# Kernel tuning notes

Measured on AMD Instinct MI355X. Metric: run time of the kernel, lower is better.

The kernel has to match this reference:

```python
import jax, jax.numpy as jnp
import numpy as np

L, B, S, D, H, V = 6, 4, 1024, 1024, 16, 32000
HD = D // H          # head_size = 64
F = 4 * D            # ffn hidden
EPS = 1e-5           # nn.LayerNorm default


def setup_inputs() -> dict:
    key = jax.random.key(0)
    ks = jax.random.split(key, 12)
    s = 0.02
    p = {
        "tokens": jax.random.randint(ks[0], (B, S), 0, V, dtype=jnp.int32),
        "tok_emb": s * jax.random.normal(ks[1], (V, D), jnp.float32),
        "pos_emb": s * jax.random.normal(ks[2], (S, D), jnp.float32),
        # stacked per-layer params (leading dim L)
        "Wq": s * jax.random.normal(ks[3], (L, D, D), jnp.float32),
        "Wk": s * jax.random.normal(ks[4], (L, D, D), jnp.float32),
        "Wv": s * jax.random.normal(ks[5], (L, D, D), jnp.float32),
        "Wp": s * jax.random.normal(ks[6], (L, D, D), jnp.float32),
        "ln1_s": jnp.ones((L, D), jnp.float32),
        "ln1_b": jnp.zeros((L, D), jnp.float32),
        "W1": s * jax.random.normal(ks[7], (L, D, F), jnp.float32),
        "b1": jnp.zeros((L, F), jnp.float32),
        "W2": s * jax.random.normal(ks[8], (L, F, D), jnp.float32),
        "b2": jnp.zeros((L, D), jnp.float32),
        "ln2_s": jnp.ones((L, D), jnp.float32),
        "ln2_b": jnp.zeros((L, D), jnp.float32),
        "lnf_s": jnp.ones((D,), jnp.float32),
        "lnf_b": jnp.zeros((D,), jnp.float32),
        "Wh": s * jax.random.normal(ks[9], (D, V), jnp.float32),
        "bh": jnp.zeros((V,), jnp.float32),
    }
    return p


def _ln(x, scale, bias):
    m = x.mean(-1, keepdims=True)
    v = ((x - m) ** 2).mean(-1, keepdims=True)
    return (x - m) * jax.lax.rsqrt(v + EPS) * scale + bias


def reference(tokens, tok_emb, pos_emb, Wq, Wk, Wv, Wp, ln1_s, ln1_b,
              W1, b1, W2, b2, ln2_s, ln2_b, lnf_s, lnf_b, Wh, bh):
    x = tok_emb[tokens] + pos_emb[None, :, :]            # [B,S,D]
    mask = jnp.tril(jnp.ones((S, S), dtype=bool))
    inv_sqrt_hd = HD ** -0.5

    def layer(x, p):
        wq, wk, wv, wp, l1s, l1b, w1, b1_, w2, b2_, l2s, l2b = p
        q = jnp.einsum('bsd,dhk->bhsk', x, wq.reshape(D, H, HD))
        k = jnp.einsum('bsd,dhk->bhsk', x, wk.reshape(D, H, HD))
        v = jnp.einsum('bsd,dhk->bhsk', x, wv.reshape(D, H, HD))
        scores = jnp.einsum('bhsk,bhtk->bhst', q, k)     # [B,H,S,S]
        # original: masked_fill(-inf) THEN * head_size**-0.5 (same math: -inf stays -inf)
        scores = jnp.where(mask, scores * inv_sqrt_hd, -jnp.inf)
        attn = jax.nn.softmax(scores, axis=-1)
        o = jnp.einsum('bhst,bhtk->bhsk', attn, v)
        o = o.transpose(0, 2, 1, 3).reshape(B, S, D) @ wp
        a = x + _ln(o, l1s, l1b)                          # residual + ln1 (as in source)
        f = jax.nn.relu(a @ w1 + b1_) @ w2 + b2_
        return x + _ln(f, l2s, l2b), None                 # residual from block INPUT (as in source)

    x, _ = jax.lax.scan(layer, x,
                        (Wq, Wk, Wv, Wp, ln1_s, ln1_b, W1, b1, W2, b2, ln2_s, ln2_b))
    return _ln(x, lnf_s, lnf_b) @ Wh + bh                 # [B,S,V]
```

## Files before the change

### kernel.cpp

```cpp
#include <hip/hip_runtime.h>

#define DEV __device__ __forceinline__

typedef __attribute__((ext_vector_type(4))) float f32x4;
typedef __attribute__((ext_vector_type(8))) short short8_t;

constexpr int LNUM = 6;
constexpr int BB = 4;
constexpr int SS = 1024;
constexpr int DD = 1024;
constexpr int HH = 16;
constexpr int HDD = 64;
constexpr int FF = 4096;
constexpr int VV = 32000;
constexpr int MROWS = BB * SS;

DEV short f2bf(float f) {
  union { float f; unsigned u; } x; x.f = f;
  unsigned r = x.u + 0x7fffu + ((x.u >> 16) & 1u);
  return (short)(r >> 16);
}

#define BAR() do { __builtin_amdgcn_sched_barrier(0); \
  __builtin_amdgcn_s_barrier(); \
  __builtin_amdgcn_sched_barrier(0); } while (0)

__global__ __launch_bounds__(256) void k_embed(
    const int* __restrict__ tok, const float* __restrict__ te,
    const float* __restrict__ pe, float* __restrict__ xf,
    short* __restrict__ xb) {
  int i = blockIdx.x * 256 + threadIdx.x;
  int bs = i >> 8, d4 = i & 255;
  int t = tok[bs];
  float4 a = ((const float4*)(te + (size_t)t * DD))[d4];
  float4 b = ((const float4*)(pe + (size_t)(bs & (SS - 1)) * DD))[d4];
  float4 r; r.x = a.x + b.x; r.y = a.y + b.y; r.z = a.z + b.z; r.w = a.w + b.w;
  ((float4*)xf)[i] = r;
  short4 o; o.x = f2bf(r.x); o.y = f2bf(r.y); o.z = f2bf(r.z); o.w = f2bf(r.w);
  ((short4*)xb)[i] = o;
}

__global__ __launch_bounds__(256) void k_tcvt(
    const float* __restrict__ in, short* __restrict__ out, int K, int N,
    long long ostride) {
  __shared__ float tile[32][33];
  const float* ip = in + (size_t)blockIdx.z * K * N;
  short* op = out + (size_t)blockIdx.z * ostride;
  int bn = blockIdx.x * 32, bk = blockIdx.y * 32;
  int tx = threadIdx.x, ty = threadIdx.y;
  #pragma unroll
  for (int r = 0; r < 32; r += 8)
    tile[ty + r][tx] = ip[(size_t)(bk + ty + r) * N + bn + tx];
  __syncthreads();
  #pragma unroll
  for (int r = 0; r < 32; r += 8)
    op[(size_t)(bn + ty + r) * K + bk + tx] = f2bf(tile[tx][ty + r]);
}

DEV void gload16(const short* g, short* l) {
  __builtin_amdgcn_global_load_lds(
      (const __attribute__((address_space(1))) void*)g,
      (__attribute__((address_space(3))) void*)l, 16, 0, 0);
}

template<int MODE>
__global__ __launch_bounds__(512, 2) void k_gemm256(
    const short* __restrict__ A, const short* __restrict__ Bt,
    const float* __restrict__ bias, void* __restrict__ Cp,
    int M, int N, int K, int lda, int ldb) {
  extern __shared__ short lds[];
  const int tid = threadIdx.x;
  const int nbx = gridDim.x;
  const int nwg = nbx << 4;
  const int hid = blockIdx.y * nbx + blockIdx.x;
  const int cpx = nwg >> 3;
  const int lid = (hid & 7) * cpx + (hid >> 3);
  const int bx = lid >> 4, by = lid & 15;
  const int n0 = bx * 256, m0 = by * 256;

  const int lane = tid & 63;
  const int wid = tid >> 6;
  const int wm = wid >> 2, wn = wid & 3;
  const int l16 = lane & 15, kg = lane >> 4;
  const int xorv = (l16 & 7) << 4;
  const int cs[2] = { ((kg << 4) ^ xorv) >> 1,
                      ((64 | (kg << 4)) ^ xorv) >> 1 };
  const int rr = tid >> 3;
  const int sce = ((((tid & 7) << 4) ^ ((rr & 7) << 4)) >> 1);
  const int ldst = (tid & ~63) * 8;

  const int NT = K >> 6;

  auto stageA = [&](int t2, int c2) {
    const int k0 = t2 << 6;
    const int base = c2 * 32768;
    #pragma unroll
    for (int h = 0; h < 2; h++)
      #pragma unroll
      for (int li = 0; li < 2; li++)
        gload16(A + (size_t)(m0 + h * 128 + li * 64 + rr) * lda + k0 + sce,
                &lds[base + h * 8192 + li * 4096 + ldst]);
  };
  auto stageB = [&](int t2, int c2) {
    const int k0 = t2 << 6;
    const int base = c2 * 32768 + 16384;
    #pragma unroll
    for (int h = 0; h < 2; h++)
      #pragma unroll
      for (int li = 0; li < 2; li++)
        gload16(Bt + (size_t)(n0 + h * 128 + li * 64 + rr) * ldb + k0 + sce,
                &lds[base + h * 8192 + li * 4096 + ldst]);
  };

  f32x4 acc[8][4];
  #pragma unroll
  for (int mi = 0; mi < 8; mi++)
    #pragma unroll
    for (int ni = 0; ni < 4; ni++)
      #pragma unroll
      for (int j = 0; j < 4; j++) acc[mi][ni][j] = 0.f;

  auto storeQ = [&](int mlo, int nlo) {
    #pragma unroll
    for (int mi = 0; mi < 4; mi++)
      #pragma unroll
      for (int ni = 0; ni < 2; ni++)
        #pragma unroll
        for (int j = 0; j < 4; j++) {
          const int r = m0 + wm * 128 + (mlo + mi) * 16 + kg * 4 + j;
          const int c = n0 + wn * 64 + (nlo + ni) * 16 + l16;
          ((float*)Cp)[(size_t)r * N + c] = acc[mlo + mi][nlo + ni][j] + bias[c];
        }
  };

  stageA(0, 0); stageB(0, 0);
  stageA(1, 1); stageB(1, 1);
  asm volatile("s_waitcnt vmcnt(8)" ::: "memory");
  BAR();

  for (int t = 0; t < NT; t++) {
    const int c = t & 1;
    const int ao = c * 32768 + wm * 8192;
    const int bo = c * 32768 + 16384 + (wn >> 1) * 8192 + (wn & 1) * 4096;
    short8_t a[4][2], b0[2][2], b1[2][2];

    #pragma unroll
    for (int mi = 0; mi < 4; mi++)
      #pragma unroll
      for (int kk = 0; kk < 2; kk++)
        a[mi][kk] = *(const short8_t*)&lds[ao + (mi * 16 + l16) * 64 + cs[kk]];
    #pragma unroll
    for (int ni = 0; ni < 2; ni++)
      #pragma unroll
      for (int kk = 0; kk < 2; kk++)
        b0[ni][kk] = *(const short8_t*)&lds[bo + (ni * 16 + l16) * 64 + cs[kk]];
    BAR();
    __builtin_amdgcn_s_setprio(1);
    #pragma unroll
    for (int mi = 0; mi < 4; mi++)
      #pragma unroll
      for (int ni = 0; ni < 2; ni++)
        #pragma unroll
        for (int kk = 0; kk < 2; kk++)
          acc[mi][ni] = __builtin_amdgcn_mfma_f32_16x16x32_bf16(
              a[mi][kk], b0[ni][kk], acc[mi][ni], 0, 0, 0);
    __builtin_amdgcn_s_setprio(0);
    if (MODE == 9 && t == NT - 1) storeQ(0, 0);
    BAR();

    #pragma unroll
    for (int ni = 0; ni < 2; ni++)
      #pragma unroll
      for (int kk = 0; kk < 2; kk++)
        b1[ni][kk] = *(const short8_t*)&lds[bo + ((ni + 2) * 16 + l16) * 64 + cs[kk]];
    BAR();
    __builtin_amdgcn_s_setprio(1);
    #pragma unroll
    for (int mi = 0; mi < 4; mi++)
      #pragma unroll
      for (int ni = 0; ni < 2; ni++)
        #pragma unroll
        for (int kk = 0; kk < 2; kk++)
          acc[mi][ni + 2] = __builtin_amdgcn_mfma_f32_16x16x32_bf16(
              a[mi][kk], b1[ni][kk], acc[mi][ni + 2], 0, 0, 0);
    __builtin_amdgcn_s_setprio(0);
    if (MODE == 9 && t == NT - 1) storeQ(0, 2);
    BAR();

    #pragma unroll
    for (int mi = 0; mi < 4; mi++)
      #pragma unroll
      for (int kk = 0; kk < 2; kk++)
        a[mi][kk] = *(const short8_t*)&lds[ao + ((mi + 4) * 16 + l16) * 64 + cs[kk]];
    if (t + 2 < NT) stageB(t + 2, c);
    BAR();
    __builtin_amdgcn_s_setprio(1);
    #pragma unroll
    for (int mi = 0; mi < 4; mi++)
      #pragma unroll
      for (int ni = 0; ni < 2; ni++)
        #pragma unroll
        for (int kk = 0; kk < 2; kk++)
          acc[mi + 4][ni + 2] = __builtin_amdgcn_mfma_f32_16x16x32_bf16(
              a[mi][kk], b1[ni][kk], acc[mi + 4][ni + 2], 0, 0, 0);
    __builtin_amdgcn_s_setprio(0);
    if (MODE == 9 && t == NT - 1) storeQ(4, 2);
    BAR();

    if (t + 2 < NT) stageA(t + 2, c);
    BAR();
    __builtin_amdgcn_s_setprio(1);
    #pragma unroll
    for (int mi = 0; mi < 4; mi++)
      #pragma unroll
      for (int ni = 0; ni < 2; ni++)
        #pragma unroll
        for (int kk = 0; kk < 2; kk++)
          acc[mi + 4][ni] = __builtin_amdgcn_mfma_f32_16x16x32_bf16(
              a[mi][kk], b0[ni][kk], acc[mi + 4][ni], 0, 0, 0);
    __builtin_amdgcn_s_setprio(0);
    if (t + 2 < NT) asm volatile("s_waitcnt vmcnt(8)" ::: "memory");
    else            asm volatile("s_waitcnt vmcnt(0)" ::: "memory");
    BAR();
  }

  if (MODE == 9) {
    storeQ(4, 0);
    return;
  }
  #pragma unroll
  for (int mi = 0; mi < 8; mi++) {
    #pragma unroll
    for (int ni = 0; ni < 4; ni++) {
      #pragma unroll
      for (int j = 0; j < 4; j++) {
        const int r = m0 + wm * 128 + mi * 16 + kg * 4 + j;
        const int c = n0 + wn * 64 + ni * 16 + l16;
        const float v = acc[mi][ni][j];
        if (MODE == 6) {
          ((short*)Cp)[(size_t)r * N + c] = f2bf(fmaxf(v + bias[c], 0.f));
        } else if (MODE == 8) {
          int kind = c >> 10, cc = c & 1023;
          int b = r >> 10, s = r & 1023, h = cc >> 6, hd = cc & 63;
          size_t off;
          if (kind < 2)
            off = (size_t)kind * MROWS * DD +
                  (((size_t)(b * HH + h) << 10) + s) * HDD + hd;
          else
            off = (size_t)2 * MROWS * DD +
                  (((size_t)(b * HH + h) * HDD + hd) << 10) + s;
          ((short*)Cp)[off] = f2bf(v);
        }
      }
    }
  }
}

template<int MODE>
__global__ __launch_bounds__(256) void k_gemm(
    const short* __restrict__ A, const short* __restrict__ Bt,
    const float* __restrict__ bias, void* __restrict__ Cp,
    int M, int N, int K, int lda, int ldb) {
  __shared__ short lA[4096];
  __shared__ short lB[4096];
  const int tid = threadIdx.x;
  const int n0 = blockIdx.x * 128, m0 = blockIdx.y * 128;

  const int lane = tid & 63;
  const int wm = (tid >> 6) >> 1, wn = (tid >> 6) & 1;
  const int l16 = lane & 15, kg = lane >> 4;
  const int srow = tid >> 2, scol = (tid & 3) * 8;
  const int lbase = (tid & ~63) * 8;

  f32x4 acc[4][4];
  #pragma unroll
  for (int a = 0; a < 4; a++)
    #pragma unroll
    for (int b = 0; b < 4; b++)
      #pragma unroll
      for (int j = 0; j < 4; j++) acc[a][b][j] = 0.f;

  for (int k0 = 0; k0 < K; k0 += 32) {
    #pragma unroll
    for (int i = 0; i < 2; i++)
      gload16(A + (size_t)(m0 + i * 64 + srow) * lda + (k0 + scol),
              &lA[i * 2048 + lbase]);
    #pragma unroll
    for (int i = 0; i < 2; i++)
      gload16(Bt + (size_t)(n0 + i * 64 + srow) * ldb + (k0 + scol),
              &lB[i * 2048 + lbase]);
    __syncthreads();
    short8_t af[4], bf[4];
    #pragma unroll
    for (int mi = 0; mi < 4; mi++)
      af[mi] = *(const short8_t*)&lA[(wm * 64 + mi * 16 + l16) * 32 + kg * 8];
    #pragma unroll
    for (int ni = 0; ni < 4; ni++)
      bf[ni] = *(const short8_t*)&lB[(wn * 64 + ni * 16 + l16) * 32 + kg * 8];
    #pragma unroll
    for (int mi = 0; mi < 4; mi++)
      #pragma unroll
      for (int ni = 0; ni < 4; ni++)
        acc[mi][ni] = __builtin_amdgcn_mfma_f32_16x16x32_bf16(
            af[mi], bf[ni], acc[mi][ni], 0, 0, 0);
    __syncthreads();
  }

  #pragma unroll
  for (int mi = 0; mi < 4; mi++) {
    #pragma unroll
    for (int ni = 0; ni < 4; ni++) {
      #pragma unroll
      for (int j = 0; j < 4; j++) {
        const int r = m0 + wm * 64 + mi * 16 + kg * 4 + j;
        const int c = n0 + wn * 64 + ni * 16 + l16;
        const float v = acc[mi][ni][j];
        if (MODE == 5) {
          ((float*)Cp)[(size_t)r * N + c] = v;
        } else if (MODE == 7) {
          ((float*)Cp)[(size_t)r * N + c] = v + bias[c];
        }
      }
    }
  }
}

#define RDSWZ(arr, r, cb) \
  (*(const short8_t*)&arr[((r) << 6) + ((((cb) ^ (((r) & 7) << 4))) >> 1)])
#define RDSWZ7(arr, r, cb) \
  (*(const short8_t*)&arr[((r) << 7) + ((((cb) ^ (((r) & 7) << 4))) >> 1)])

__global__ __launch_bounds__(512, 2) void k_attn(
    const short* __restrict__ Qg, const short* __restrict__ Kgl,
    const short* __restrict__ Vt, short* __restrict__ Og) {
  extern __shared__ short sm[];
  short* lP = sm + 32768;
  const int tid = threadIdx.x;
  const int z = blockIdx.y;
  const int qb = (z < 32) ? blockIdx.x : 7 - blockIdx.x;
  const int q0 = qb << 7;
  const short* Qp = Qg + ((size_t)z << 16);
  const short* Kp = Kgl + ((size_t)z << 16);
  const short* Vp = Vt + ((size_t)z << 16);
  const int bidx = z >> 4, h = z & 15;
  const int lane = tid & 63, w = tid >> 6;
  const int l16 = lane & 15, kg = lane >> 4;
  const int sr = tid >> 3;
  const int scb = ((((tid & 7) << 4) ^ ((sr & 7) << 4)) >> 1);
  const int vr = tid >> 4;
  const int vcb = ((((tid & 15) << 4) ^ ((vr & 7) << 4)) >> 1);
  const int ldst = (tid & ~63) << 3;

  auto stageK = [&](int kt, int c) {
    const int k0 = kt << 7;
    short* dst = sm + c * 16384;
    #pragma unroll
    for (int i = 0; i < 2; i++)
      gload16(Kp + ((size_t)(k0 + i * 64 + sr) << 6) + scb,
              dst + i * 4096 + ldst);
  };
  auto stageV = [&](int kt, int c) {
    const int k0 = kt << 7;
    short* dst = sm + c * 16384 + 8192;
    #pragma unroll
    for (int i = 0; i < 2; i++)
      gload16(Vp + ((size_t)(i * 32 + vr) << 10) + k0 + vcb,
              dst + i * 4096 + ldst);
  };

  #pragma unroll
  for (int i = 0; i < 2; i++)
    gload16(Qp + ((size_t)(q0 + i * 64 + sr) << 6) + scb,
            sm + 16384 + i * 4096 + ldst);
  __syncthreads();
  short8_t aq[2];
  #pragma unroll
  for (int kk = 0; kk < 2; kk++)
    aq[kk] = RDSWZ((sm + 16384), w * 16 + l16, kk * 64 + kg * 16);
  __syncthreads();

  f32x4 acc_o[4];
  float m_r[4], l_r[4];
  #pragma unroll
  for (int j = 0; j < 4; j++) {
    m_r[j] = -3e38f; l_r[j] = 0.f;
    #pragma unroll
    for (int n2 = 0; n2 < 4; n2++) acc_o[n2][j] = 0.f;
  }

  const float C = 0.125f * 1.44269504f;
  const int nkt = qb + 1;
  stageK(0, 0); stageV(0, 0);

  for (int kt = 0; kt < nkt; kt++) {
    const int cur = kt & 1;
    if (kt + 1 < nkt) {
      stageK(kt + 1, cur ^ 1); stageV(kt + 1, cur ^ 1);
      asm volatile("s_waitcnt vmcnt(4)" ::: "memory");
    } else {
      asm volatile("s_waitcnt vmcnt(0)" ::: "memory");
    }
    BAR();

    const short* lK = sm + cur * 16384;
    const short* lV = sm + cur * 16384 + 8192;
    const int k0 = kt << 7;

    f32x4 s[8];
    #pragma unroll
    for (int nf = 0; nf < 8; nf++)
      #pragma unroll
      for (int j = 0; j < 4; j++) s[nf][j] = 0.f;
    #pragma unroll
    for (int kk = 0; kk < 2; kk++)
      #pragma unroll
      for (int nf = 0; nf < 8; nf++) {
        short8_t bk = RDSWZ(lK, nf * 16 + l16, kk * 64 + kg * 16);
        s[nf] = __builtin_amdgcn_mfma_f32_16x16x32_bf16(aq[kk], bk, s[nf], 0, 0, 0);
      }

    const bool diag = (kt == qb);
    #pragma unroll
    for (int j = 0; j < 4; j++) {
      const int ql = w * 16 + kg * 4 + j;
      const int q = q0 + ql;
      float sv[8]; float tm = -3e38f;
      #pragma unroll
      for (int nf = 0; nf < 8; nf++) {
        const int kv = k0 + nf * 16 + l16;
        const float x = s[nf][j] * C;
        sv[nf] = (!diag || kv <= q) ? x : -3e38f;
        tm = fmaxf(tm, sv[nf]);
      }
      #pragma unroll
      for (int o = 1; o < 16; o <<= 1) tm = fmaxf(tm, __shfl_xor(tm, o));
      const float mn = fmaxf(m_r[j], tm);
      const float scale = exp2f(m_r[j] - mn);
      float ts = 0.f;
      #pragma unroll
      for (int nf = 0; nf < 8; nf++) {
        const float e = exp2f(sv[nf] - mn);
        ts += e;
        lP[(ql << 7) + ((nf * 16 + l16) ^ ((ql & 7) << 3))] = f2bf(e);
      }
      #pragma unroll
      for (int o = 1; o < 16; o <<= 1) ts += __shfl_xor(ts, o);
      l_r[j] = l_r[j] * scale + ts;
      m_r[j] = mn;
      #pragma unroll
      for (int n2 = 0; n2 < 4; n2++) acc_o[n2][j] *= scale;
    }

    #pragma unroll
    for (int kc = 0; kc < 4; kc++) {
      const int pr = w * 16 + l16;
      short8_t pa = *(const short8_t*)
          &lP[(pr << 7) + ((kc * 32 + kg * 8) ^ ((pr & 7) << 3))];
      #pragma unroll
      for (int n2 = 0; n2 < 4; n2++) {
        short8_t vb = RDSWZ7(lV, n2 * 16 + l16, kc * 64 + kg * 16);
        acc_o[n2] = __builtin_amdgcn_mfma_f32_16x16x32_bf16(pa, vb, acc_o[n2], 0, 0, 0);
      }
    }
    BAR();
  }

  #pragma unroll
  for (int j = 0; j < 4; j++) {
    const int q = q0 + w * 16 + kg * 4 + j;
    const float inv = 1.f / l_r[j];
    #pragma unroll
    for (int n2 = 0; n2 < 4; n2++) {
      const int col = h * HDD + n2 * 16 + l16;
      Og[(((size_t)bidx << 10) + q) * DD + col] = f2bf(acc_o[n2][j] * inv);
    }
  }
}

template<int ADD_RES, int WRITE_F32>
__global__ __launch_bounds__(256) void k_ln(
    const float* __restrict__ src, const float* __restrict__ res,
    const float* __restrict__ g, const float* __restrict__ b,
    float* __restrict__ of, short* __restrict__ ob) {
  const int row = blockIdx.x;
  const int tid = threadIdx.x;
  float4 v = ((const float4*)(src + ((size_t)row << 10)))[tid];
  float s1 = v.x + v.y + v.z + v.w;
  float s2 = v.x * v.x + v.y * v.y + v.z * v.z + v.w * v.w;
  #pragma unroll
  for (int o = 32; o; o >>= 1) { s1 += __shfl_xor(s1, o); s2 += __shfl_xor(s2, o); }
  __shared__ float sh1[4], sh2[4];
  if ((tid & 63) == 0) { sh1[tid >> 6] = s1; sh2[tid >> 6] = s2; }
  __syncthreads();
  s1 = sh1[0] + sh1[1] + sh1[2] + sh1[3];
  s2 = sh2[0] + sh2[1] + sh2[2] + sh2[3];
  const float mean = s1 * (1.f / 1024.f);
  const float var  = s2 * (1.f / 1024.f) - mean * mean;
  const float rs = rsqrtf(var + 1e-5f);
  float4 gg = ((const float4*)g)[tid];
  float4 bb = ((const float4*)b)[tid];
  float4 o4;
  o4.x = (v.x - mean) * rs * gg.x + bb.x;
  o4.y = (v.y - mean) * rs * gg.y + bb.y;
  o4.z = (v.z - mean) * rs * gg.z + bb.z;
  o4.w = (v.w - mean) * rs * gg.w + bb.w;
  if (ADD_RES) {
    float4 rr = ((const float4*)(res + ((size_t)row << 10)))[tid];
    o4.x += rr.x; o4.y += rr.y; o4.z += rr.z; o4.w += rr.w;
  }
  if (WRITE_F32) ((float4*)(of + ((size_t)row << 10)))[tid] = o4;
  short4 s4; s4.x = f2bf(o4.x); s4.y = f2bf(o4.y);
  s4.z = f2bf(o4.z); s4.w = f2bf(o4.w);
  ((short4*)ob)[((size_t)row << 8) + tid] = s4;
}

extern "C" void kernel_launch(void* const* d_in, const int* in_sizes, int n_in,
                              void* d_out, int out_size, void* d_ws, size_t ws_size,
                              hipStream_t stream) {
  (void)in_sizes; (void)n_in; (void)out_size; (void)ws_size;
  const int*   tokens  = (const int*)d_in[0];
  const float* tok_emb = (const float*)d_in[1];
  const float* pos_emb = (const float*)d_in[2];
  const float* Wq = (const float*)d_in[3];
  const float* Wk = (const float*)d_in[4];
  const float* Wv = (const float*)d_in[5];
  const float* Wp = (const float*)d_in[6];
  const float* ln1s = (const float*)d_in[7];
  const float* ln1b = (const float*)d_in[8];
  const float* W1 = (const float*)d_in[9];
  const float* b1 = (const float*)d_in[10];
  const float* W2 = (const float*)d_in[11];
  const float* b2 = (const float*)d_in[12];
  const float* ln2s = (const float*)d_in[13];
  const float* ln2b = (const float*)d_in[14];
  const float* lnfs = (const float*)d_in[15];
  const float* lnfb = (const float*)d_in[16];
  const float* Wh = (const float*)d_in[17];
  const float* bh = (const float*)d_in[18];
  float* out = (float*)d_out;

  hipFuncSetAttribute((const void*)k_gemm256<6>,
      hipFuncAttributeMaxDynamicSharedMemorySize, 131072);
  hipFuncSetAttribute((const void*)k_gemm256<8>,
      hipFuncAttributeMaxDynamicSharedMemorySize, 131072);
  hipFuncSetAttribute((const void*)k_gemm256<9>,
      hipFuncAttributeMaxDynamicSharedMemorySize, 131072);
  hipFuncSetAttribute((const void*)k_attn,
      hipFuncAttributeMaxDynamicSharedMemorySize, 98304);

  char* p = (char*)d_ws;
  auto alloc = [&](size_t elems, size_t esz) -> char* {
    char* r = p; p += (elems * esz + 255) & ~(size_t)255; return r;
  };
  short* WqkvT = (short*)alloc((size_t)LNUM * 3 * DD * DD, 2);
  short* WpT = (short*)alloc((size_t)LNUM * DD * DD, 2);
  short* W1T = (short*)alloc((size_t)LNUM * DD * FF, 2);
  short* W2T = (short*)alloc((size_t)LNUM * DD * FF, 2);
  short* WhT = (short*)alloc((size_t)DD * VV, 2);
  float* xf   = (float*)alloc((size_t)MROWS * DD, 4);
  float* ff   = (float*)alloc((size_t)MROWS * DD, 4);
  short* xb   = (short*)alloc((size_t)MROWS * DD, 2);
  short* ab   = (short*)alloc((size_t)MROWS * DD, 2);
  short* qkvb = (short*)alloc((size_t)3 * MROWS * DD, 2);
  short* obuf = (short*)alloc((size_t)MROWS * DD, 2);
  short* hb   = (short*)alloc((size_t)MROWS * FF, 2);
  short* xfb  = (short*)alloc((size_t)MROWS * DD, 2);
  short* qb   = qkvb;
  short* kb   = qkvb + (size_t)MROWS * DD;
  short* vtb  = qkvb + (size_t)2 * MROWS * DD;

  dim3 blk(256);
  dim3 t8(32, 8);
  const long long DD2 = (long long)DD * DD;
  k_tcvt<<<dim3(DD / 32, DD / 32, LNUM), t8, 0, stream>>>(Wq, WqkvT,          DD, DD, 3 * DD2);
  k_tcvt<<<dim3(DD / 32, DD / 32, LNUM), t8, 0, stream>>>(Wk, WqkvT + DD2,    DD, DD, 3 * DD2);
  k_tcvt<<<dim3(DD / 32, DD / 32, LNUM), t8, 0, stream>>>(Wv, WqkvT + 2*DD2,  DD, DD, 3 * DD2);
  k_tcvt<<<dim3(DD / 32, DD / 32, LNUM), t8, 0, stream>>>(Wp, WpT, DD, DD, DD2);
  k_tcvt<<<dim3(FF / 32, DD / 32, LNUM), t8, 0, stream>>>(W1, W1T, DD, FF, (long long)DD * FF);
  k_tcvt<<<dim3(DD / 32, FF / 32, LNUM), t8, 0, stream>>>(W2, W2T, FF, DD, (long long)DD * FF);
  k_tcvt<<<dim3(VV / 32, DD / 32, 1),   t8, 0, stream>>>(Wh, WhT, DD, VV, 0);

  k_embed<<<(MROWS * DD / 4) / 256, blk, 0, stream>>>(tokens, tok_emb, pos_emb, xf, xb);

  for (int l = 0; l < LNUM; l++) {
    const short* wqkv = WqkvT + (size_t)l * 3 * DD * DD;
    const short* wp = WpT + (size_t)l * DD * DD;
    const short* w1 = W1T + (size_t)l * DD * FF;
    const short* w2 = W2T + (size_t)l * DD * FF;

    k_gemm256<8><<<dim3(12, 16), 512, 131072, stream>>>(xb, wqkv, nullptr, qkvb,
        MROWS, 3 * DD, DD, DD, DD);
    k_attn<<<dim3(8, BB * HH), 512, 98304, stream>>>(qb, kb, vtb, obuf);
    k_gemm<5><<<dim3(8, 32), blk, 0, stream>>>(obuf, wp, nullptr, ff,
        MROWS, DD, DD, DD, DD);
    k_ln<1, 0><<<MROWS, blk, 0, stream>>>(ff, xf, ln1s + (size_t)l * DD,
        ln1b + (size_t)l * DD, nullptr, ab);
    k_gemm256<6><<<dim3(16, 16), 512, 131072, stream>>>(ab, w1, b1 + (size_t)l * FF, hb,
        MROWS, FF, DD, DD, DD);
    k_gemm<7><<<dim3(8, 32), blk, 0, stream>>>(hb, w2, b2 + (size_t)l * DD, ff,
        MROWS, DD, FF, FF, FF);
    k_ln<1, 1><<<MROWS, blk, 0, stream>>>(ff, xf, ln2s + (size_t)l * DD,
        ln2b + (size_t)l * DD, xf, xb);
  }

  k_ln<0, 0><<<MROWS, blk, 0, stream>>>(xf, nullptr, lnfs, lnfb, nullptr, xfb);
  k_gemm256<9><<<dim3(VV / 256, 16), 512, 131072, stream>>>(xfb, WhT, bh, out,
      MROWS, VV, DD, DD, DD);
}
```

Before: 2.398 ms.

## Replace 256x256 GEMM with 256x128 tile, BK=32 kernel for more occupancy

Replaces the 256x256-tile, K=64, four-phase interleaved GEMM with a simpler 256x128 tile over 32-wide K steps. It uses one combined A/B stage per iteration and 48KB of LDS, so up to four blocks can fit per CU. The grids for the QKV, FFN1 and LM-head GEMMs double, which improves wave balance on the many CUs. The cost is lower arithmetic intensity per tile, more barriers per unit of K, and loss of the fine-grained load/MFMA interleaving. It also merges the three Q/K/V weight transpose launches into one kernel.

```diff
diff --git a/kernel.cpp b/kernel.cpp
--- a/kernel.cpp
+++ b/kernel.cpp
@@ -57,6 +57,25 @@
     op[(size_t)(bn + ty + r) * K + bk + tx] = f2bf(tile[tx][ty + r]);
 }
 
+__global__ __launch_bounds__(256) void k_tcvt3(
+    const float* __restrict__ Wq, const float* __restrict__ Wk,
+    const float* __restrict__ Wv, short* __restrict__ out) {
+  __shared__ float tile[32][33];
+  const int z = blockIdx.z, l = z / 3, which = z - l * 3;
+  const float* ip = (which == 0 ? Wq : which == 1 ? Wk : Wv)
+                    + (size_t)l * DD * DD;
+  short* op = out + ((size_t)l * 3 + which) * DD * DD;
+  int bn = blockIdx.x * 32, bk = blockIdx.y * 32;
+  int tx = threadIdx.x, ty = threadIdx.y;
+  #pragma unroll
+  for (int r = 0; r < 32; r += 8)
+    tile[ty + r][tx] = ip[(size_t)(bk + ty + r) * DD + bn + tx];
+  __syncthreads();
+  #pragma unroll
+  for (int r = 0; r < 32; r += 8)
+    op[(size_t)(bn + ty + r) * DD + bk + tx] = f2bf(tile[tx][ty + r]);
+}
+
 DEV void gload16(const short* g, short* l) {
   __builtin_amdgcn_global_load_lds(
       (const __attribute__((address_space(1))) void*)g,
@@ -64,7 +83,7 @@
 }
 
 template<int MODE>
-__global__ __launch_bounds__(512, 2) void k_gemm256(
+__global__ __launch_bounds__(512, 4) void k_g2(
     const short* __restrict__ A, const short* __restrict__ Bt,
     const float* __restrict__ bias, void* __restrict__ Cp,
     int M, int N, int K, int lda, int ldb) {
@@ -76,169 +95,81 @@
   const int cpx = nwg >> 3;
   const int lid = (hid & 7) * cpx + (hid >> 3);
   const int bx = lid >> 4, by = lid & 15;
-  const int n0 = bx * 256, m0 = by * 256;
+  const int n0 = bx * 128, m0 = by * 256;
 
   const int lane = tid & 63;
   const int wid = tid >> 6;
-  const int wm = wid >> 2, wn = wid & 3;
+  const int wm = wid >> 1, wn = wid & 1;
   const int l16 = lane & 15, kg = lane >> 4;
-  const int xorv = (l16 & 7) << 4;
-  const int cs[2] = { ((kg << 4) ^ xorv) >> 1,
-                      ((64 | (kg << 4)) ^ xorv) >> 1 };
-  const int rr = tid >> 3;
-  const int sce = ((((tid & 7) << 4) ^ ((rr & 7) << 4)) >> 1);
+  const int cso = ((kg << 4) ^ ((l16 & 3) << 4)) >> 1;
+  const int rr = tid >> 2;
+  const int sce = ((((tid & 3) << 4) ^ ((rr & 3) << 4)) >> 1);
   const int ldst = (tid & ~63) * 8;
 
-  const int NT = K >> 6;
-
-  auto stageA = [&](int t2, int c2) {
-    const int k0 = t2 << 6;
-    const int base = c2 * 32768;
+  const int NT = K >> 5;
+
+  auto stage = [&](int t2, int c) {
+    const int k0 = t2 << 5;
     #pragma unroll
     for (int h = 0; h < 2; h++)
-      #pragma unroll
-      for (int li = 0; li < 2; li++)
-        gload16(A + (size_t)(m0 + h * 128 + li * 64 + rr) * lda + k0 + sce,
-                &lds[base + h * 8192 + li * 4096 + ldst]);
+      gload16(A + (size_t)(m0 + h * 128 + rr) * lda + k0 + sce,
+              &lds[c * 12288 + h * 4096 + ldst]);
+    gload16(Bt + (size_t)(n0 + rr) * ldb + k0 + sce,
+            &lds[c * 12288 + 8192 + ldst]);
   };
-  auto stageB = [&](int t2, int c2) {
-    const int k0 = t2 << 6;
-    const int base = c2 * 32768 + 16384;
-    #pragma unroll
-    for (int h = 0; h < 2; h++)
-      #pragma unroll
-      for (int li = 0; li < 2; li++)
-        gload16(Bt + (size_t)(n0 + h * 128 + li * 64 + rr) * ldb + k0 + sce,
-                &lds[base + h * 8192 + li * 4096 + ldst]);
-  };
-
-  f32x4 acc[8][4];
-  #pragma unroll
-  for (int mi = 0; mi < 8; mi++)
+
+  f32x4 acc[4][4];
+  #pragma unroll
+  for (int mi = 0; mi < 4; mi++)
     #pragma unroll
     for (int ni = 0; ni < 4; ni++)
       #pragma unroll
       for (int j = 0; j < 4; j++) acc[mi][ni][j] = 0.f;
 
-  auto storeQ = [&](int mlo, int nlo) {
-    #pragma unroll
-    for (int mi = 0; mi < 4; mi++)
-      #pragma unroll
-      for (int ni = 0; ni < 2; ni++)
-        #pragma unroll
-        for (int j = 0; j < 4; j++) {
-          const int r = m0 + wm * 128 + (mlo + mi) * 16 + kg * 4 + j;
-          const int c = n0 + wn * 64 + (nlo + ni) * 16 + l16;
-          ((float*)Cp)[(size_t)r * N + c] = acc[mlo + mi][nlo + ni][j] + bias[c];
-        }
-  };
-
-  stageA(0, 0); stageB(0, 0);
-  stageA(1, 1); stageB(1, 1);
-  asm volatile("s_waitcnt vmcnt(8)" ::: "memory");
+  stage(0, 0); stage(1, 1);
+  asm volatile("s_waitcnt vmcnt(3)" ::: "memory");
   BAR();
 
   for (int t = 0; t < NT; t++) {
     const int c = t & 1;
-    const int ao = c * 32768 + wm * 8192;
-    const int bo = c * 32768 + 16384 + (wn >> 1) * 8192 + (wn & 1) * 4096;
-    short8_t a[4][2], b0[2][2], b1[2][2];
-
+    const int ab = c * 12288;
+    short8_t a[4], b[4];
     #pragma unroll
     for (int mi = 0; mi < 4; mi++)
-      #pragma unroll
-      for (int kk = 0; kk < 2; kk++)
-        a[mi][kk] = *(const short8_t*)&lds[ao + (mi * 16 + l16) * 64 + cs[kk]];
-    #pragma unroll
-    for (int ni = 0; ni < 2; ni++)
-      #pragma unroll
-      for (int kk = 0; kk < 2; kk++)
-        b0[ni][kk] = *(const short8_t*)&lds[bo + (ni * 16 + l16) * 64 + cs[kk]];
+      a[mi] = *(const short8_t*)&lds[ab + (wm * 64 + mi * 16 + l16) * 32 + cso];
+    #pragma unroll
+    for (int ni = 0; ni < 4; ni++)
+      b[ni] = *(const short8_t*)&lds[ab + 8192 + (wn * 64 + ni * 16 + l16) * 32 + cso];
+    asm volatile("s_waitcnt lgkmcnt(0)" ::: "memory");
+    __builtin_amdgcn_sched_barrier(0);
     BAR();
+    if (t + 2 < NT) stage(t + 2, c);
     __builtin_amdgcn_s_setprio(1);
     #pragma unroll
     for (int mi = 0; mi < 4; mi++)
       #pragma unroll
-      for (int ni = 0; ni < 2; ni++)
-        #pragma unroll
-        for (int kk = 0; kk < 2; kk++)
-          acc[mi][ni] = __builtin_amdgcn_mfma_f32_16x16x32_bf16(
-              a[mi][kk], b0[ni][kk], acc[mi][ni], 0, 0, 0);
+      for (int ni = 0; ni < 4; ni++)
+        acc[mi][ni] = __builtin_amdgcn_mfma_f32_16x16x32_bf16(
+            a[mi], b[ni], acc[mi][ni], 0, 0, 0);
     __builtin_amdgcn_s_setprio(0);
-    if (MODE == 9 && t == NT - 1) storeQ(0, 0);
+    if (t + 2 < NT)      asm volatile("s_waitcnt vmcnt(3)" ::: "memory");
+    else if (t + 1 < NT) asm volatile("s_waitcnt vmcnt(0)" ::: "memory");
     BAR();
-
-    #pragma unroll
-    for (int ni = 0; ni < 2; ni++)
-      #pragma unroll
-      for (int kk = 0; kk < 2; kk++)
-        b1[ni][kk] = *(const short8_t*)&lds[bo + ((ni + 2) * 16 + l16) * 64 + cs[kk]];
-    BAR();
-    __builtin_amdgcn_s_setprio(1);
-    #pragma unroll
-    for (int mi = 0; mi < 4; mi++)
-      #pragma unroll
-      for (int ni = 0; ni < 2; ni++)
-        #pragma unroll
-        for (int kk = 0; kk < 2; kk++)
-          acc[mi][ni + 2] = __builtin_amdgcn_mfma_f32_16x16x32_bf16(
-              a[mi][kk], b1[ni][kk], acc[mi][ni + 2], 0, 0, 0);
-    __builtin_amdgcn_s_setprio(0);
-    if (MODE == 9 && t == NT - 1) storeQ(0, 2);
-    BAR();
-
-    #pragma unroll
-    for (int mi = 0; mi < 4; mi++)
-      #pragma unroll
-      for (int kk = 0; kk < 2; kk++)
-        a[mi][kk] = *(const short8_t*)&lds[ao + ((mi + 4) * 16 + l16) * 64 + cs[kk]];
-    if (t + 2 < NT) stageB(t + 2, c);
-    BAR();
-    __builtin_amdgcn_s_setprio(1);
-    #pragma unroll
-    for (int mi = 0; mi < 4; mi++)
-      #pragma unroll
-      for (int ni = 0; ni < 2; ni++)
-        #pragma unroll
-        for (int kk = 0; kk < 2; kk++)
-          acc[mi + 4][ni + 2] = __builtin_amdgcn_mfma_f32_16x16x32_bf16(
-              a[mi][kk], b1[ni][kk], acc[mi + 4][ni + 2], 0, 0, 0);
-    __builtin_amdgcn_s_setprio(0);
-    if (MODE == 9 && t == NT - 1) storeQ(4, 2);
-    BAR();
-
-    if (t + 2 < NT) stageA(t + 2, c);
-    BAR();
-    __builtin_amdgcn_s_setprio(1);
-    #pragma unroll
-    for (int mi = 0; mi < 4; mi++)
-      #pragma unroll
-      for (int ni = 0; ni < 2; ni++)
-        #pragma unroll
-        for (int kk = 0; kk < 2; kk++)
-          acc[mi + 4][ni] = __builtin_amdgcn_mfma_f32_16x16x32_bf16(
-              a[mi][kk], b0[ni][kk], acc[mi + 4][ni], 0, 0, 0);
-    __builtin_amdgcn_s_setprio(0);
-    if (t + 2 < NT) asm volatile("s_waitcnt vmcnt(8)" ::: "memory");
-    else            asm volatile("s_waitcnt vmcnt(0)" ::: "memory");
-    BAR();
-  }
-
-  if (MODE == 9) {
-    storeQ(4, 0);
-    return;
-  }
-  #pragma unroll
-  for (int mi = 0; mi < 8; mi++) {
+  }
+
+  #pragma unroll
+  for (int mi = 0; mi < 4; mi++) {
     #pragma unroll
     for (int ni = 0; ni < 4; ni++) {
       #pragma unroll
       for (int j = 0; j < 4; j++) {
-        const int r = m0 + wm * 128 + mi * 16 + kg * 4 + j;
+        const int r = m0 + wm * 64 + mi * 16 + kg * 4 + j;
         const int c = n0 + wn * 64 + ni * 16 + l16;
         const float v = acc[mi][ni][j];
         if (MODE == 6) {
           ((short*)Cp)[(size_t)r * N + c] = f2bf(fmaxf(v + bias[c], 0.f));
+        } else if (MODE == 9) {
+          ((float*)Cp)[(size_t)r * N + c] = v + bias[c];
         } else if (MODE == 8) {
           int kind = c >> 10, cc = c & 1023;
           int b = r >> 10, s = r & 1023, h = cc >> 6, hd = cc & 63;
@@ -539,12 +470,12 @@
   const float* bh = (const float*)d_in[18];
   float* out = (float*)d_out;
 
-  hipFuncSetAttribute((const void*)k_gemm256<6>,
-      hipFuncAttributeMaxDynamicSharedMemorySize, 131072);
-  hipFuncSetAttribute((const void*)k_gemm256<8>,
-      hipFuncAttributeMaxDynamicSharedMemorySize, 131072);
-  hipFuncSetAttribute((const void*)k_gemm256<9>,
-      hipFuncAttributeMaxDynamicSharedMemorySize, 131072);
+  hipFuncSetAttribute((const void*)k_g2<6>,
+      hipFuncAttributeMaxDynamicSharedMemorySize, 49152);
+  hipFuncSetAttribute((const void*)k_g2<8>,
+      hipFuncAttributeMaxDynamicSharedMemorySize, 49152);
+  hipFuncSetAttribute((const void*)k_g2<9>,
+      hipFuncAttributeMaxDynamicSharedMemorySize, 49152);
   hipFuncSetAttribute((const void*)k_attn,
       hipFuncAttributeMaxDynamicSharedMemorySize, 98304);
 
@@ -571,13 +502,13 @@
 
   dim3 blk(256);
   dim3 t8(32, 8);
-  const long long DD2 = (long long)DD * DD;
-  k_tcvt<<<dim3(DD / 32, DD / 32, LNUM), t8, 0, stream>>>(Wq, WqkvT,          DD, DD, 3 * DD2);
-  k_tcvt<<<dim3(DD / 32, DD / 32, LNUM), t8, 0, stream>>>(Wk, WqkvT + DD2,    DD, DD, 3 * DD2);
-  k_tcvt<<<dim3(DD / 32, DD / 32, LNUM), t8, 0, stream>>>(Wv, WqkvT + 2*DD2,  DD, DD, 3 * DD2);
-  k_tcvt<<<dim3(DD / 32, DD / 32, LNUM), t8, 0, stream>>>(Wp, WpT, DD, DD, DD2);
-  k_tcvt<<<dim3(FF / 32, DD / 32, LNUM), t8, 0, stream>>>(W1, W1T, DD, FF, (long long)DD * FF);
-  k_tcvt<<<dim3(DD / 32, FF / 32, LNUM), t8, 0, stream>>>(W2, W2T, FF, DD, (long long)DD * FF);
+  k_tcvt3<<<dim3(DD / 32, DD / 32, 3 * LNUM), t8, 0, stream>>>(Wq, Wk, Wv, WqkvT);
+  k_tcvt<<<dim3(DD / 32, DD / 32, LNUM), t8, 0, stream>>>(Wp, WpT, DD, DD,
+      (long long)DD * DD);
+  k_tcvt<<<dim3(FF / 32, DD / 32, LNUM), t8, 0, stream>>>(W1, W1T, DD, FF,
+      (long long)DD * FF);
+  k_tcvt<<<dim3(DD / 32, FF / 32, LNUM), t8, 0, stream>>>(W2, W2T, FF, DD,
+      (long long)DD * FF);
   k_tcvt<<<dim3(VV / 32, DD / 32, 1),   t8, 0, stream>>>(Wh, WhT, DD, VV, 0);
 
   k_embed<<<(MROWS * DD / 4) / 256, blk, 0, stream>>>(tokens, tok_emb, pos_emb, xf, xb);
@@ -588,14 +519,14 @@
     const short* w1 = W1T + (size_t)l * DD * FF;
     const short* w2 = W2T + (size_t)l * DD * FF;
 
-    k_gemm256<8><<<dim3(12, 16), 512, 131072, stream>>>(xb, wqkv, nullptr, qkvb,
+    k_g2<8><<<dim3(24, 16), 512, 49152, stream>>>(xb, wqkv, nullptr, qkvb,
         MROWS, 3 * DD, DD, DD, DD);
     k_attn<<<dim3(8, BB * HH), 512, 98304, stream>>>(qb, kb, vtb, obuf);
     k_gemm<5><<<dim3(8, 32), blk, 0, stream>>>(obuf, wp, nullptr, ff,
         MROWS, DD, DD, DD, DD);
     k_ln<1, 0><<<MROWS, blk, 0, stream>>>(ff, xf, ln1s + (size_t)l * DD,
         ln1b + (size_t)l * DD, nullptr, ab);
-    k_gemm256<6><<<dim3(16, 16), 512, 131072, stream>>>(ab, w1, b1 + (size_t)l * FF, hb,
+    k_g2<6><<<dim3(32, 16), 512, 49152, stream>>>(ab, w1, b1 + (size_t)l * FF, hb,
         MROWS, FF, DD, DD, DD);
     k_gemm<7><<<dim3(8, 32), blk, 0, stream>>>(hb, w2, b2 + (size_t)l * DD, ff,
         MROWS, DD, FF, FF, FF);
@@ -604,6 +535,6 @@
   }
 
   k_ln<0, 0><<<MROWS, blk, 0, stream>>>(xf, nullptr, lnfs, lnfb, nullptr, xfb);
-  k_gemm256<9><<<dim3(VV / 256, 16), 512, 131072, stream>>>(xfb, WhT, bh, out,
+  k_g2<9><<<dim3(VV / 128, 16), 512, 49152, stream>>>(xfb, WhT, bh, out,
       MROWS, VV, DD, DD, DD);
 }
```

Measured after the change: 2.401 ms. Within noise of the previous version (+0.1%).
